# Optimization experiments

Hardware: AMD Instinct MI355X
Metric: run time of the kernel (lower is better)

Reference implementation:

```python
import jax, jax.numpy as jnp
import numpy as np

B, T, D, H = 4, 2048, 1024, 16
HD = D // H  # head_dim = 64

def setup_inputs() -> dict:
    key = jax.random.key(0)
    k1, k2, k3 = jax.random.split(key, 3)
    x = jax.random.normal(k1, (B, T, D), dtype=jnp.float32)
    w_qkv = jax.random.normal(k2, (D, 3 * D), dtype=jnp.float32) * (D ** -0.5)
    b_qkv = jnp.zeros((3 * D,), dtype=jnp.float32)
    w_proj = jax.random.normal(k3, (D, D), dtype=jnp.float32) * (D ** -0.5)
    b_proj = jnp.zeros((D,), dtype=jnp.float32)
    return {"x": x, "w_qkv": w_qkv, "b_qkv": b_qkv, "w_proj": w_proj, "b_proj": b_proj}

def reference(x, w_qkv, b_qkv, w_proj, b_proj):
    b, t, d = x.shape
    scale = HD ** -0.5
    qkv = x @ w_qkv + b_qkv                          # [B,T,3D]
    qkv = qkv.reshape(b, t, 3, H, HD)
    qkv = jnp.transpose(qkv, (2, 0, 3, 1, 4))        # [3,B,H,T,HD]
    q, k, v = qkv[0], qkv[1], qkv[2]
    att = jnp.einsum("bhqd,bhkd->bhqk", q, k) * scale  # [B,H,T,T]
    mask = jnp.tril(jnp.ones((t, t), dtype=att.dtype))[None, None]
    att = att * mask + (1.0 - mask) * (-1e9)
    att = jax.nn.softmax(att, axis=-1)
    # dropout inactive (training=False)
    y = jnp.einsum("bhqk,bhkd->bhqd", att, v)        # [B,H,T,HD]
    y = jnp.transpose(y, (0, 2, 1, 3)).reshape(b, t, d)
    return y @ w_proj + b_proj
```

## Files before the change

### kernel.cpp

```cpp
#include <hip/hip_runtime.h>
#include <hip/hip_bf16.h>

typedef unsigned short u16;
typedef short short8 __attribute__((ext_vector_type(8)));
typedef short bf16x4 __attribute__((ext_vector_type(4)));
typedef float f32x4 __attribute__((ext_vector_type(4)));
typedef float f32x16 __attribute__((ext_vector_type(16)));

#define B_SZ 4
#define T_SEQ 2048
#define DMODEL 1024
#define NH 16
#define HD 64
#define QKV_ELEMS 8388608ull
#define QSCALE (0.125f * 1.44269504f)

__device__ __forceinline__ u16 f2bf(float f) {
    __hip_bfloat16 h = __float2bfloat16(f);
    return __builtin_bit_cast(u16, h);
}

__device__ __forceinline__ void gload16(const void* g, void* l) {
    __builtin_amdgcn_global_load_lds(
        (const __attribute__((address_space(1))) unsigned int*)g,
        (__attribute__((address_space(3))) unsigned int*)l, 16, 0, 0);
}

__global__ __launch_bounds__(256) void cast_x_kernel(
    const float4* __restrict__ x, u16* __restrict__ xb)
{
    const int i = blockIdx.x * 256 + threadIdx.x;
    const float4 v = x[i];
    union { u16 u[4]; uint2 d; } p;
    p.u[0] = f2bf(v.x); p.u[1] = f2bf(v.y); p.u[2] = f2bf(v.z); p.u[3] = f2bf(v.w);
    *(uint2*)(xb + (size_t)i * 4) = p.d;
}

__global__ __launch_bounds__(256) void tcast_kernel(
    const float* __restrict__ w, u16* __restrict__ wt, int K, int N)
{
    const int n = blockIdx.x * 256 + threadIdx.x;
    const int k0 = blockIdx.y * 256;
    for (int kk = 0; kk < 256; kk += 8) {
        short8 o;
#pragma unroll
        for (int e = 0; e < 8; ++e)
            o[e] = (short)f2bf(w[(size_t)(k0 + kk + e) * N + n]);
        *(short8*)&wt[(size_t)n * K + k0 + kk] = o;
    }
}

template <int EPI>
__global__ __launch_bounds__(256) void gemm_kernel(
    const u16* __restrict__ A, const u16* __restrict__ Bt,
    const float* __restrict__ bias, void* __restrict__ outp)
{
    __shared__ u16 As[128 * 64];
    __shared__ u16 Bs[128 * 64];
    const int tid = threadIdx.x;
    const int l = tid & 63;
    const int w = tid >> 6;
    const int wm = w >> 1, wn = w & 1;
    const int m0 = blockIdx.y * 128, n0 = blockIdx.x * 128;
    const int srow = l >> 3;
    const int sch  = (l & 7) ^ srow;
    const int fr = l & 15, fq = l >> 4;

    f32x4 acc[4][4] = {};

    for (int k0 = 0; k0 < 1024; k0 += 64) {
        __syncthreads();
#pragma unroll
        for (int ii = 0; ii < 4; ++ii) {
            const int row = w * 32 + ii * 8;
            gload16(&A[(size_t)(m0 + row + srow) * 1024 + k0 + sch * 8], &As[row * 64]);
            gload16(&Bt[(size_t)(n0 + row + srow) * 1024 + k0 + sch * 8], &Bs[row * 64]);
        }
        __syncthreads();
#pragma unroll
        for (int ks = 0; ks < 2; ++ks) {
            short8 af[4], bf[4];
#pragma unroll
            for (int t = 0; t < 4; ++t) {
                const int ar = wm * 64 + t * 16 + fr;
                af[t] = *(const short8*)&As[ar * 64 + (((ks * 4 + fq) ^ (l & 7)) << 3)];
                const int br = wn * 64 + t * 16 + fr;
                bf[t] = *(const short8*)&Bs[br * 64 + (((ks * 4 + fq) ^ (l & 7)) << 3)];
            }
#pragma unroll
            for (int mt = 0; mt < 4; ++mt)
#pragma unroll
                for (int nt = 0; nt < 4; ++nt)
                    acc[mt][nt] = __builtin_amdgcn_mfma_f32_16x16x32_bf16(
                        af[mt], bf[nt], acc[mt][nt], 0, 0, 0);
        }
    }

    if (EPI == 0) {
        u16* qkv = (u16*)outp;
#pragma unroll
        for (int nt = 0; nt < 4; ++nt) {
            const int n = n0 + wn * 64 + nt * 16 + fr;
            const float bs = bias[n];
            const int which = n >> 10, hh = (n >> 6) & 15, d = n & 63;
            if (which == 2) {
                u16* dst = qkv + 2 * QKV_ELEMS;
#pragma unroll
                for (int mt = 0; mt < 4; ++mt) {
                    const int m = m0 + wm * 64 + mt * 16 + fq * 4;
                    const int bb = m >> 11, t = m & 2047;
                    bf16x4 ov;
#pragma unroll
                    for (int r = 0; r < 4; ++r) ov[r] = (short)f2bf(acc[mt][nt][r] + bs);
                    *(bf16x4*)&dst[(((size_t)(bb * NH + hh)) * HD + d) * T_SEQ + t] = ov;
                }
            } else {
                const float scl = (which == 0) ? QSCALE : 1.0f;
                u16* dst = qkv + (size_t)which * QKV_ELEMS + (size_t)hh * T_SEQ * HD + d;
#pragma unroll
                for (int mt = 0; mt < 4; ++mt)
#pragma unroll
                    for (int r = 0; r < 4; ++r) {
                        const int m = m0 + wm * 64 + mt * 16 + fq * 4 + r;
                        const int bb = m >> 11, t = m & 2047;
                        dst[(size_t)bb * (NH * T_SEQ * HD) + (size_t)t * HD] =
                            f2bf((acc[mt][nt][r] + bs) * scl);
                    }
            }
        }
    } else {
        float* C = (float*)outp;
#pragma unroll
        for (int nt = 0; nt < 4; ++nt) {
            const int n = n0 + wn * 64 + nt * 16 + fr;
            const float bs = bias[n];
#pragma unroll
            for (int mt = 0; mt < 4; ++mt)
#pragma unroll
                for (int r = 0; r < 4; ++r) {
                    const int m = m0 + wm * 64 + mt * 16 + fq * 4 + r;
                    C[(size_t)m * DMODEL + n] = acc[mt][nt][r] + bs;
                }
        }
    }
}

__global__ __launch_bounds__(256) void attn_kernel(
    const u16* __restrict__ q, const u16* __restrict__ k,
    const u16* __restrict__ vT, u16* __restrict__ y)
{
    __shared__ u16 Ks[2][64 * 64];
    __shared__ u16 Vs[2][64 * 64];

    const int flat = blockIdx.x;
    const int f0 = flat & 1, f8 = (flat >> 8) & 1;
    const int j4 = ((flat >> 6) & 8) | ((flat >> 1) & 7);
    const int qi = (f0 ^ f8) ? (15 - j4) : j4;
    const int hh = (flat >> 4) & 15;
    const int bb = ((flat >> 7) & 2) | f0;

    const int q0 = qi * 128;
    const size_t hbase = ((size_t)(bb * NH + hh)) * T_SEQ * HD;
    const u16* qb = q + hbase;
    const u16* kb = k + hbase;
    const u16* vTb = vT + hbase;

    const int tid = threadIdx.x;
    const int l = tid & 63;
    const int w = tid >> 6;
    const int qn = l & 31;
    const int h = l >> 5;
    const int srow = l >> 3;
    const int sch = (l & 7) ^ srow;

    u16* Qstage = &Ks[0][0];

#pragma unroll
    for (int ii = 0; ii < 4; ++ii) {
        const int row = w * 32 + ii * 8;
        gload16(&qb[(size_t)(q0 + row + srow) * HD + sch * 8], &Qstage[row * 64]);
    }
    {
        const int row = w * 16, row2 = w * 16 + 8;
        gload16(&vTb[(size_t)(row + srow) * T_SEQ + sch * 8], &Vs[0][row * 64]);
        gload16(&vTb[(size_t)(row2 + srow) * T_SEQ + sch * 8], &Vs[0][row2 * 64]);
    }
    __syncthreads();

    short8 qf[4];
    {
        const int qrow = w * 32 + qn;
#pragma unroll
        for (int k16 = 0; k16 < 4; ++k16)
            qf[k16] = *(const short8*)
                &Qstage[qrow * 64 + (((k16 * 2 + h) ^ (qrow & 7)) << 3)];
    }
    __syncthreads();

    {
        const int row = w * 16, row2 = w * 16 + 8;
        gload16(&kb[(size_t)(row + srow) * HD + sch * 8], &Ks[0][row * 64]);
        gload16(&kb[(size_t)(row2 + srow) * HD + sch * 8], &Ks[0][row2 * 64]);
    }

    const int q0w = q0 + w * 32;
    float m_run = -1e30f, l_run = 0.f;
    f32x16 o_acc[2] = {};

    const int nkt = 2 * (qi + 1);
    for (int kt = 0; kt < nkt; ++kt) {
        __syncthreads();
        if (kt + 1 < nkt) {
            const int nb = (kt + 1) & 1;
            const int jj = (kt + 1) * 64;
            const int row = w * 16, row2 = w * 16 + 8;
            gload16(&kb[(size_t)(jj + row + srow) * HD + sch * 8], &Ks[nb][row * 64]);
            gload16(&kb[(size_t)(jj + row2 + srow) * HD + sch * 8], &Ks[nb][row2 * 64]);
            gload16(&vTb[(size_t)(row + srow) * T_SEQ + jj + sch * 8], &Vs[nb][row * 64]);
            gload16(&vTb[(size_t)(row2 + srow) * T_SEQ + jj + sch * 8], &Vs[nb][row2 * 64]);
        }
        const int buf = kt & 1;
        const int j0 = kt * 64;

        if (j0 > q0w + 31) continue;
        const int njt = (j0 + 32 <= q0w + 31) ? 2 : 1;

        f32x16 st[2];
#pragma unroll
        for (int jt = 0; jt < 2; ++jt) {
            if (jt >= njt) continue;
            f32x16 s = {};
#pragma unroll
            for (int k16 = 0; k16 < 4; ++k16) {
                const int jrow = jt * 32 + qn;
                const short8 kf = *(const short8*)
                    &Ks[buf][jrow * 64 + (((k16 * 2 + h) ^ (jrow & 7)) << 3)];
                s = __builtin_amdgcn_mfma_f32_32x32x16_bf16(kf, qf[k16], s, 0, 0, 0);
            }
            st[jt] = s;
        }

        const int qg = q0w + qn;
        float pmax = -3.0e38f;
#pragma unroll
        for (int jt = 0; jt < 2; ++jt) {
            if (jt >= njt) continue;
            const bool needMask = (j0 + jt * 32 + 31) > q0w;
            if (needMask) {
#pragma unroll
                for (int r = 0; r < 16; ++r) {
                    const int jg = j0 + jt * 32 + (r & 3) + 8 * (r >> 2) + 4 * h;
                    if (jg > qg) st[jt][r] = -1e30f;
                }
            }
#pragma unroll
            for (int r = 0; r < 16; ++r) pmax = fmaxf(pmax, st[jt][r]);
        }
        pmax = fmaxf(pmax, __shfl_xor(pmax, 32));

        if (!__all(pmax - m_run <= 8.0f)) {
            const float mxn = fmaxf(m_run, pmax);
            const float alpha = exp2f(m_run - mxn);
            m_run = mxn;
            l_run *= alpha;
#pragma unroll
            for (int dt = 0; dt < 2; ++dt)
#pragma unroll
                for (int r = 0; r < 16; ++r) o_acc[dt][r] *= alpha;
        }

        float ls = 0.f;
#pragma unroll
        for (int jt = 0; jt < 2; ++jt) {
            if (jt >= njt) continue;
#pragma unroll
            for (int r = 0; r < 16; ++r) {
                const float p = exp2f(st[jt][r] - m_run);
                st[jt][r] = p;
                ls += p;
            }
        }
        ls += __shfl_xor(ls, 32);
        l_run += ls;

#pragma unroll
        for (int jt = 0; jt < 2; ++jt) {
            if (jt >= njt) continue;
#pragma unroll
            for (int g = 0; g < 4; ++g) {
                bf16x4 pk;
#pragma unroll
                for (int e = 0; e < 4; ++e) pk[e] = (short)f2bf(st[jt][g * 4 + e]);
#pragma unroll
                for (int dt = 0; dt < 2; ++dt) {
                    const int drow = dt * 32 + qn;
                    const bf16x4 vf = *(const bf16x4*)
                        &Vs[buf][drow * 64 +
                                 (((jt * 4 + g) ^ (drow & 7)) << 3) + h * 4];
                    o_acc[dt] = __builtin_amdgcn_mfma_f32_32x32x8bf16_1k(
                        vf, pk, o_acc[dt], 0, 0, 0);
                }
            }
        }
    }

    const float inv = 1.f / l_run;
    const int t = q0w + qn;
    u16* yrow = y + ((size_t)(bb * T_SEQ + t)) * DMODEL + hh * HD;
#pragma unroll
    for (int dt = 0; dt < 2; ++dt)
#pragma unroll
        for (int g = 0; g < 4; ++g) {
            bf16x4 ov;
#pragma unroll
            for (int e = 0; e < 4; ++e)
                ov[e] = (short)f2bf(o_acc[dt][g * 4 + e] * inv);
            *(bf16x4*)&yrow[dt * 32 + g * 8 + h * 4] = ov;
        }
}

extern "C" void kernel_launch(void* const* d_in, const int* in_sizes, int n_in,
                              void* d_out, int out_size, void* d_ws, size_t ws_size,
                              hipStream_t stream) {
    const float* x      = (const float*)d_in[0];
    const float* w_qkv  = (const float*)d_in[1];
    const float* b_qkv  = (const float*)d_in[2];
    const float* w_proj = (const float*)d_in[3];
    const float* b_proj = (const float*)d_in[4];
    float* out = (float*)d_out;

    u16* xb  = (u16*)d_ws;
    u16* wqT = xb + 8388608;
    u16* wpT = wqT + 3145728;
    u16* qkv = wpT + 1048576;
    u16* yb  = qkv + 3 * QKV_ELEMS;

    cast_x_kernel<<<8192, 256, 0, stream>>>((const float4*)x, xb);
    tcast_kernel<<<dim3(12, 4), 256, 0, stream>>>(w_qkv, wqT, 1024, 3072);
    tcast_kernel<<<dim3(4, 4), 256, 0, stream>>>(w_proj, wpT, 1024, 1024);
    gemm_kernel<0><<<dim3(24, 64), 256, 0, stream>>>(xb, wqT, b_qkv, (void*)qkv);
    attn_kernel<<<dim3(1024), 256, 0, stream>>>(
        qkv, qkv + QKV_ELEMS, qkv + 2 * QKV_ELEMS, yb);
    gemm_kernel<1><<<dim3(8, 64), 256, 0, stream>>>(yb, wpT, b_proj, (void*)out);
}
```

Before: 319.2 us.

## Pair causal query tiles per attention block and remap workgroups across XCDs

The attention kernel now launches half as many blocks, and each block handles two query tiles (qi and 15-qi) in sequence, so every block does the same amount of causal work. Workgroup IDs in both the attention and GEMM kernels are remapped in strides of 8, so neighbouring tiles land on the same XCD and can share L2 cache. The softmax max and sum reductions are split into independent partial accumulators to shorten dependency chains. The trade-off is fewer blocks in flight, with each block running longer and serially, which may lower occupancy and overlap.

Result: slower. 326.1 us (+2.2%).

```diff
diff --git a/kernel.cpp b/kernel.cpp
--- a/kernel.cpp
+++ b/kernel.cpp
@@ -61,7 +61,12 @@
     const int l = tid & 63;
     const int w = tid >> 6;
     const int wm = w >> 1, wn = w & 1;
-    const int m0 = blockIdx.y * 128, n0 = blockIdx.x * 128;
+
+    const int nwg = gridDim.x * gridDim.y;
+    int flat = blockIdx.y * gridDim.x + blockIdx.x;
+    flat = (flat & 7) * (nwg >> 3) + (flat >> 3);
+    const int m0 = (flat / gridDim.x) * 128, n0 = (flat % gridDim.x) * 128;
+
     const int srow = l >> 3;
     const int sch  = (l & 7) ^ srow;
     const int fr = l & 15, fq = l >> 4;
@@ -152,14 +157,12 @@
     __shared__ u16 Ks[2][64 * 64];
     __shared__ u16 Vs[2][64 * 64];
 
-    const int flat = blockIdx.x;
-    const int f0 = flat & 1, f8 = (flat >> 8) & 1;
-    const int j4 = ((flat >> 6) & 8) | ((flat >> 1) & 7);
-    const int qi = (f0 ^ f8) ? (15 - j4) : j4;
-    const int hh = (flat >> 4) & 15;
-    const int bb = ((flat >> 7) & 2) | f0;
-
-    const int q0 = qi * 128;
+    int flat = blockIdx.x;
+    flat = (flat & 7) * 64 + (flat >> 3);
+    const int qip = flat & 7;
+    const int hh = (flat >> 3) & 15;
+    const int bb = flat >> 7;
+
     const size_t hbase = ((size_t)(bb * NH + hh)) * T_SEQ * HD;
     const u16* qb = q + hbase;
     const u16* kb = k + hbase;
@@ -175,148 +178,166 @@
 
     u16* Qstage = &Ks[0][0];
 
-#pragma unroll
-    for (int ii = 0; ii < 4; ++ii) {
-        const int row = w * 32 + ii * 8;
-        gload16(&qb[(size_t)(q0 + row + srow) * HD + sch * 8], &Qstage[row * 64]);
+    for (int pp = 0; pp < 2; ++pp) {
+        const int qi = pp ? (15 - qip) : qip;
+        const int q0 = qi * 128;
+
+        __syncthreads();
+
+#pragma unroll
+        for (int ii = 0; ii < 4; ++ii) {
+            const int row = w * 32 + ii * 8;
+            gload16(&qb[(size_t)(q0 + row + srow) * HD + sch * 8], &Qstage[row * 64]);
+        }
+        {
+            const int row = w * 16, row2 = w * 16 + 8;
+            gload16(&vTb[(size_t)(row + srow) * T_SEQ + sch * 8], &Vs[0][row * 64]);
+            gload16(&vTb[(size_t)(row2 + srow) * T_SEQ + sch * 8], &Vs[0][row2 * 64]);
+        }
+        __syncthreads();
+
+        short8 qf[4];
+        {
+            const int qrow = w * 32 + qn;
+#pragma unroll
+            for (int k16 = 0; k16 < 4; ++k16)
+                qf[k16] = *(const short8*)
+                    &Qstage[qrow * 64 + (((k16 * 2 + h) ^ (qrow & 7)) << 3)];
+        }
+        __syncthreads();
+
+        {
+            const int row = w * 16, row2 = w * 16 + 8;
+            gload16(&kb[(size_t)(row + srow) * HD + sch * 8], &Ks[0][row * 64]);
+            gload16(&kb[(size_t)(row2 + srow) * HD + sch * 8], &Ks[0][row2 * 64]);
+        }
+
+        const int q0w = q0 + w * 32;
+        float m_run = -1e30f, l_run = 0.f;
+        f32x16 o_acc[2] = {};
+
+        const int nkt = 2 * (qi + 1);
+        for (int kt = 0; kt < nkt; ++kt) {
+            __syncthreads();
+            if (kt + 1 < nkt) {
+                const int nb = (kt + 1) & 1;
+                const int jj = (kt + 1) * 64;
+                const int row = w * 16, row2 = w * 16 + 8;
+                gload16(&kb[(size_t)(jj + row + srow) * HD + sch * 8],
+                        &Ks[nb][row * 64]);
+                gload16(&kb[(size_t)(jj + row2 + srow) * HD + sch * 8],
+                        &Ks[nb][row2 * 64]);
+                gload16(&vTb[(size_t)(row + srow) * T_SEQ + jj + sch * 8],
+                        &Vs[nb][row * 64]);
+                gload16(&vTb[(size_t)(row2 + srow) * T_SEQ + jj + sch * 8],
+                        &Vs[nb][row2 * 64]);
+            }
+            const int buf = kt & 1;
+            const int j0 = kt * 64;
+
+            if (j0 > q0w + 31) continue;
+            const int njt = (j0 + 32 <= q0w + 31) ? 2 : 1;
+
+            f32x16 st[2];
+#pragma unroll
+            for (int jt = 0; jt < 2; ++jt) {
+                if (jt >= njt) continue;
+                f32x16 s = {};
+#pragma unroll
+                for (int k16 = 0; k16 < 4; ++k16) {
+                    const int jrow = jt * 32 + qn;
+                    const short8 kf = *(const short8*)
+                        &Ks[buf][jrow * 64 + (((k16 * 2 + h) ^ (jrow & 7)) << 3)];
+                    s = __builtin_amdgcn_mfma_f32_32x32x16_bf16(kf, qf[k16], s, 0, 0, 0);
+                }
+                st[jt] = s;
+            }
+
+            const int qg = q0w + qn;
+            float pmax = -3.0e38f;
+#pragma unroll
+            for (int jt = 0; jt < 2; ++jt) {
+                if (jt >= njt) continue;
+                const bool needMask = (j0 + jt * 32 + 31) > q0w;
+                if (needMask) {
+#pragma unroll
+                    for (int r = 0; r < 16; ++r) {
+                        const int jg = j0 + jt * 32 + (r & 3) + 8 * (r >> 2) + 4 * h;
+                        if (jg > qg) st[jt][r] = -1e30f;
+                    }
+                }
+#pragma unroll
+                for (int r = 0; r < 16; r += 2)
+                    pmax = fmaxf(pmax, fmaxf(st[jt][r], st[jt][r + 1]));
+            }
+            pmax = fmaxf(pmax, __shfl_xor(pmax, 32));
+
+            if (!__all(pmax - m_run <= 8.0f)) {
+                const float mxn = fmaxf(m_run, pmax);
+                const float alpha = exp2f(m_run - mxn);
+                m_run = mxn;
+                l_run *= alpha;
+#pragma unroll
+                for (int dt = 0; dt < 2; ++dt)
+#pragma unroll
+                    for (int r = 0; r < 16; ++r) o_acc[dt][r] *= alpha;
+            }
+
+            float ls = 0.f;
+#pragma unroll
+            for (int jt = 0; jt < 2; ++jt) {
+                if (jt >= njt) continue;
+                float s0 = 0.f, s1 = 0.f, s2 = 0.f, s3 = 0.f;
+#pragma unroll
+                for (int r = 0; r < 16; r += 4) {
+                    float p0 = exp2f(st[jt][r] - m_run);
+                    float p1 = exp2f(st[jt][r + 1] - m_run);
+                    float p2 = exp2f(st[jt][r + 2] - m_run);
+                    float p3 = exp2f(st[jt][r + 3] - m_run);
+                    st[jt][r] = p0; st[jt][r + 1] = p1;
+                    st[jt][r + 2] = p2; st[jt][r + 3] = p3;
+                    s0 += p0; s1 += p1; s2 += p2; s3 += p3;
+                }
+                ls += (s0 + s1) + (s2 + s3);
+            }
+            ls += __shfl_xor(ls, 32);
+            l_run += ls;
+
+#pragma unroll
+            for (int jt = 0; jt < 2; ++jt) {
+                if (jt >= njt) continue;
+#pragma unroll
+                for (int g = 0; g < 4; ++g) {
+                    bf16x4 pk;
+#pragma unroll
+                    for (int e = 0; e < 4; ++e) pk[e] = (short)f2bf(st[jt][g * 4 + e]);
+#pragma unroll
+                    for (int dt = 0; dt < 2; ++dt) {
+                        const int drow = dt * 32 + qn;
+                        const bf16x4 vf = *(const bf16x4*)
+                            &Vs[buf][drow * 64 +
+                                     (((jt * 4 + g) ^ (drow & 7)) << 3) + h * 4];
+                        o_acc[dt] = __builtin_amdgcn_mfma_f32_32x32x8bf16_1k(
+                            vf, pk, o_acc[dt], 0, 0, 0);
+                    }
+                }
+            }
+        }
+
+        const float inv = 1.f / l_run;
+        const int t = q0w + qn;
+        u16* yrow = y + ((size_t)(bb * T_SEQ + t)) * DMODEL + hh * HD;
+#pragma unroll
+        for (int dt = 0; dt < 2; ++dt)
+#pragma unroll
+            for (int g = 0; g < 4; ++g) {
+                bf16x4 ov;
+#pragma unroll
+                for (int e = 0; e < 4; ++e)
+                    ov[e] = (short)f2bf(o_acc[dt][g * 4 + e] * inv);
+                *(bf16x4*)&yrow[dt * 32 + g * 8 + h * 4] = ov;
+            }
     }
-    {
-        const int row = w * 16, row2 = w * 16 + 8;
-        gload16(&vTb[(size_t)(row + srow) * T_SEQ + sch * 8], &Vs[0][row * 64]);
-        gload16(&vTb[(size_t)(row2 + srow) * T_SEQ + sch * 8], &Vs[0][row2 * 64]);
-    }
-    __syncthreads();
-
-    short8 qf[4];
-    {
-        const int qrow = w * 32 + qn;
-#pragma unroll
-        for (int k16 = 0; k16 < 4; ++k16)
-            qf[k16] = *(const short8*)
-                &Qstage[qrow * 64 + (((k16 * 2 + h) ^ (qrow & 7)) << 3)];
-    }
-    __syncthreads();
-
-    {
-        const int row = w * 16, row2 = w * 16 + 8;
-        gload16(&kb[(size_t)(row + srow) * HD + sch * 8], &Ks[0][row * 64]);
-        gload16(&kb[(size_t)(row2 + srow) * HD + sch * 8], &Ks[0][row2 * 64]);
-    }
-
-    const int q0w = q0 + w * 32;
-    float m_run = -1e30f, l_run = 0.f;
-    f32x16 o_acc[2] = {};
-
-    const int nkt = 2 * (qi + 1);
-    for (int kt = 0; kt < nkt; ++kt) {
-        __syncthreads();
-        if (kt + 1 < nkt) {
-            const int nb = (kt + 1) & 1;
-            const int jj = (kt + 1) * 64;
-            const int row = w * 16, row2 = w * 16 + 8;
-            gload16(&kb[(size_t)(jj + row + srow) * HD + sch * 8], &Ks[nb][row * 64]);
-            gload16(&kb[(size_t)(jj + row2 + srow) * HD + sch * 8], &Ks[nb][row2 * 64]);
-            gload16(&vTb[(size_t)(row + srow) * T_SEQ + jj + sch * 8], &Vs[nb][row * 64]);
-            gload16(&vTb[(size_t)(row2 + srow) * T_SEQ + jj + sch * 8], &Vs[nb][row2 * 64]);
-        }
-        const int buf = kt & 1;
-        const int j0 = kt * 64;
-
-        if (j0 > q0w + 31) continue;
-        const int njt = (j0 + 32 <= q0w + 31) ? 2 : 1;
-
-        f32x16 st[2];
-#pragma unroll
-        for (int jt = 0; jt < 2; ++jt) {
-            if (jt >= njt) continue;
-            f32x16 s = {};
-#pragma unroll
-            for (int k16 = 0; k16 < 4; ++k16) {
-                const int jrow = jt * 32 + qn;
-                const short8 kf = *(const short8*)
-                    &Ks[buf][jrow * 64 + (((k16 * 2 + h) ^ (jrow & 7)) << 3)];
-                s = __builtin_amdgcn_mfma_f32_32x32x16_bf16(kf, qf[k16], s, 0, 0, 0);
-            }
-            st[jt] = s;
-        }
-
-        const int qg = q0w + qn;
-        float pmax = -3.0e38f;
-#pragma unroll
-        for (int jt = 0; jt < 2; ++jt) {
-            if (jt >= njt) continue;
-            const bool needMask = (j0 + jt * 32 + 31) > q0w;
-            if (needMask) {
-#pragma unroll
-                for (int r = 0; r < 16; ++r) {
-                    const int jg = j0 + jt * 32 + (r & 3) + 8 * (r >> 2) + 4 * h;
-                    if (jg > qg) st[jt][r] = -1e30f;
-                }
-            }
-#pragma unroll
-            for (int r = 0; r < 16; ++r) pmax = fmaxf(pmax, st[jt][r]);
-        }
-        pmax = fmaxf(pmax, __shfl_xor(pmax, 32));
-
-        if (!__all(pmax - m_run <= 8.0f)) {
-            const float mxn = fmaxf(m_run, pmax);
-            const float alpha = exp2f(m_run - mxn);
-            m_run = mxn;
-            l_run *= alpha;
-#pragma unroll
-            for (int dt = 0; dt < 2; ++dt)
-#pragma unroll
-                for (int r = 0; r < 16; ++r) o_acc[dt][r] *= alpha;
-        }
-
-        float ls = 0.f;
-#pragma unroll
-        for (int jt = 0; jt < 2; ++jt) {
-            if (jt >= njt) continue;
-#pragma unroll
-            for (int r = 0; r < 16; ++r) {
-                const float p = exp2f(st[jt][r] - m_run);
-                st[jt][r] = p;
-                ls += p;
-            }
-        }
-        ls += __shfl_xor(ls, 32);
-        l_run += ls;
-
-#pragma unroll
-        for (int jt = 0; jt < 2; ++jt) {
-            if (jt >= njt) continue;
-#pragma unroll
-            for (int g = 0; g < 4; ++g) {
-                bf16x4 pk;
-#pragma unroll
-                for (int e = 0; e < 4; ++e) pk[e] = (short)f2bf(st[jt][g * 4 + e]);
-#pragma unroll
-                for (int dt = 0; dt < 2; ++dt) {
-                    const int drow = dt * 32 + qn;
-                    const bf16x4 vf = *(const bf16x4*)
-                        &Vs[buf][drow * 64 +
-                                 (((jt * 4 + g) ^ (drow & 7)) << 3) + h * 4];
-                    o_acc[dt] = __builtin_amdgcn_mfma_f32_32x32x8bf16_1k(
-                        vf, pk, o_acc[dt], 0, 0, 0);
-                }
-            }
-        }
-    }
-
-    const float inv = 1.f / l_run;
-    const int t = q0w + qn;
-    u16* yrow = y + ((size_t)(bb * T_SEQ + t)) * DMODEL + hh * HD;
-#pragma unroll
-    for (int dt = 0; dt < 2; ++dt)
-#pragma unroll
-        for (int g = 0; g < 4; ++g) {
-            bf16x4 ov;
-#pragma unroll
-            for (int e = 0; e < 4; ++e)
-                ov[e] = (short)f2bf(o_acc[dt][g * 4 + e] * inv);
-            *(bf16x4*)&yrow[dt * 32 + g * 8 + h * 4] = ov;
-        }
 }
 
 extern "C" void kernel_launch(void* const* d_in, const int* in_sizes, int n_in,
@@ -339,7 +360,7 @@
     tcast_kernel<<<dim3(12, 4), 256, 0, stream>>>(w_qkv, wqT, 1024, 3072);
     tcast_kernel<<<dim3(4, 4), 256, 0, stream>>>(w_proj, wpT, 1024, 1024);
     gemm_kernel<0><<<dim3(24, 64), 256, 0, stream>>>(xb, wqT, b_qkv, (void*)qkv);
-    attn_kernel<<<dim3(1024), 256, 0, stream>>>(
+    attn_kernel<<<dim3(512), 256, 0, stream>>>(
         qkv, qkv + QKV_ELEMS, qkv + 2 * QKV_ELEMS, yb);
     gemm_kernel<1><<<dim3(8, 64), 256, 0, stream>>>(yb, wpT, b_proj, (void*)out);
 }
```
